# Optimization experiments

Measured on AMD Instinct MI355X. Metric: run time of the kernel, lower is better.

Reference implementation:

```python
import jax, jax.numpy as jnp
import numpy as np

N_NODES = 40000
N_EDGES = 320000
IN_DIM = 256
HID = 128
HEADS = 4
N_GAT = 3  # num_layers - 1
EPS = 1e-5
NEG_SLOPE = 0.2  # PyG GATConv default


def setup_inputs() -> dict:
    key = jax.random.key(0)
    ks = jax.random.split(key, 16)
    s = 0.05
    return {
        "x": jax.random.normal(ks[0], (N_NODES, IN_DIM), jnp.float32),
        "edge_index": jax.random.randint(ks[1], (2, N_EDGES), 0, N_NODES, jnp.int64),
        "proj_W": jax.random.normal(ks[2], (IN_DIM, HID), jnp.float32) * s,
        "proj_b": jnp.zeros((HID,), jnp.float32),
        "gat_W": jax.random.normal(ks[3], (N_GAT, HID, HEADS * HID), jnp.float32) * s,
        "gat_att_src": jax.random.normal(ks[4], (N_GAT, HEADS, HID), jnp.float32) * s,
        "gat_att_dst": jax.random.normal(ks[5], (N_GAT, HEADS, HID), jnp.float32) * s,
        "gat_bias": jnp.zeros((N_GAT, HID), jnp.float32),
        "ln_gamma": jnp.ones((N_GAT, HID), jnp.float32),
        "ln_beta": jnp.zeros((N_GAT, HID), jnp.float32),
        "gcn_W": jax.random.normal(ks[6], (HID, 1), jnp.float32) * s,
        "gcn_b": jnp.zeros((1,), jnp.float32),
    }


def reference(x, edge_index, proj_W, proj_b, gat_W, gat_att_src, gat_att_dst,
              gat_bias, ln_gamma, ln_beta, gcn_W, gcn_b):
    N = x.shape[0]
    loops = jnp.arange(N)
    src = jnp.concatenate([edge_index[0], loops])  # add_self_loops=True
    dst = jnp.concatenate([edge_index[1], loops])

    h = x @ proj_W + proj_b  # [N, HID]

    for i in range(N_GAT):
        identity = h
        xh = (h @ gat_W[i]).reshape(N, HEADS, HID)      # [N, H, C]
        a_s = jnp.einsum("nhc,hc->nh", xh, gat_att_src[i])  # [N, H]
        a_d = jnp.einsum("nhc,hc->nh", xh, gat_att_dst[i])
        e = jax.nn.leaky_relu(a_s[src] + a_d[dst], NEG_SLOPE)  # [E, H]
        # segment softmax over incoming edges per dst node
        m = jax.ops.segment_max(e, dst, num_segments=N)
        ex = jnp.exp(e - m[dst])
        denom = jax.ops.segment_sum(ex, dst, num_segments=N)
        alpha = ex / denom[dst]                         # [E, H]
        agg = jax.ops.segment_sum(xh[src] * alpha[:, :, None], dst, num_segments=N)
        h = agg.mean(axis=1) + gat_bias[i]              # concat=False -> head mean
        # LayerNorm (biased variance, eps=1e-5)
        mu = h.mean(-1, keepdims=True)
        var = ((h - mu) ** 2).mean(-1, keepdims=True)
        h = (h - mu) * jax.lax.rsqrt(var + EPS) * ln_gamma[i] + ln_beta[i]
        h = jax.nn.relu(h)
        # dropout: inference mode -> identity
        h = h + identity

    # GCNConv(hidden, 1) with symmetric normalization and self loops
    deg = jax.ops.segment_sum(jnp.ones_like(dst, dtype=h.dtype), dst, num_segments=N)
    dinv = jax.lax.rsqrt(deg)  # deg >= 1 due to self loops
    norm = dinv[src] * dinv[dst]                        # [E]
    xw = h @ gcn_W                                      # [N, 1]
    out = jax.ops.segment_sum(xw[src] * norm[:, None], dst, num_segments=N) + gcn_b
    return jax.nn.sigmoid(out).reshape(-1)
```

## Files before the change

### kernel.cpp

```cpp
#include <hip/hip_runtime.h>
#include <math.h>

#define INDIM 256
#define HID 128
#define HEADS 4
#define NGAT 3
#define LN_EPS 1e-5f
#define SLOPE 0.2f
#define MPAD 40064
#define LOG2E 1.4426950408889634f

typedef __attribute__((ext_vector_type(8))) short short8;
typedef __attribute__((ext_vector_type(4))) float f32x4;

__device__ inline float wsum(float v) {
#pragma unroll
  for (int m = 1; m < 64; m <<= 1) v += __shfl_xor(v, m, 64);
  return v;
}
__device__ inline float wmax(float v) {
#pragma unroll
  for (int m = 1; m < 64; m <<= 1) v = fmaxf(v, __shfl_xor(v, m, 64));
  return v;
}
__device__ inline float lk2(float v) { return fmaxf(v, SLOPE * v) * LOG2E; }
__device__ inline float sel4(float a0, float a1, float a2, float a3, int i) {
  float lo = (i & 1) ? a1 : a0;
  float hi = (i & 1) ? a3 : a2;
  return (i & 2) ? hi : lo;
}

__device__ inline unsigned short f2b(float f) {
  unsigned u = __float_as_uint(f);
  unsigned r = (u + 0x7FFFu + ((u >> 16) & 1u)) >> 16;
  return (unsigned short)r;
}
__device__ inline float b2f(unsigned short b) {
  return __uint_as_float(((unsigned)b) << 16);
}
__device__ inline void unp8(const uint4 v, float f[8]) {
  f[0] = __uint_as_float(v.x << 16);
  f[1] = __uint_as_float(v.x & 0xFFFF0000u);
  f[2] = __uint_as_float(v.y << 16);
  f[3] = __uint_as_float(v.y & 0xFFFF0000u);
  f[4] = __uint_as_float(v.z << 16);
  f[5] = __uint_as_float(v.z & 0xFFFF0000u);
  f[6] = __uint_as_float(v.w << 16);
  f[7] = __uint_as_float(v.w & 0xFFFF0000u);
}

__device__ __host__ inline size_t fidx(int row, int k, int K) {
  return ((size_t)(row >> 4) * (K >> 5) + (k >> 5)) * 512 +
         ((((k >> 3) & 3) * 16 + (row & 15)) << 3) + (k & 7);
}

__global__ void k_deg(const int* __restrict__ ei, int E, int N, int* __restrict__ deg) {
  int e = blockIdx.x * blockDim.x + threadIdx.x;
  if (e >= E + N) return;
  int dst = (e < E) ? ei[E + e] : (e - E);
  atomicAdd(&deg[dst], 1);
}

__global__ void k_scan1(const int* __restrict__ deg, int N, int* __restrict__ bsums) {
  __shared__ int s[256];
  int gid = blockIdx.x * 256 + threadIdx.x;
  s[threadIdx.x] = (gid < N) ? deg[gid] : 0;
  __syncthreads();
  for (int off = 128; off > 0; off >>= 1) {
    if (threadIdx.x < off) s[threadIdx.x] += s[threadIdx.x + off];
    __syncthreads();
  }
  if (threadIdx.x == 0) bsums[blockIdx.x] = s[0];
}

__global__ void k_scan2(int* __restrict__ bsums, int nblk, int* __restrict__ rowptr, int N) {
  __shared__ int s[256];
  int t = threadIdx.x;
  int v = (t < nblk) ? bsums[t] : 0;
  s[t] = v;
  __syncthreads();
  for (int off = 1; off < 256; off <<= 1) {
    int u = (t >= off) ? s[t - off] : 0;
    __syncthreads();
    s[t] += u;
    __syncthreads();
  }
  if (t < nblk) bsums[t] = s[t] - v;
  if (t == nblk - 1) rowptr[N] = s[t];
}

__global__ void k_scan3(const int* __restrict__ deg, int N, const int* __restrict__ bsums,
                        int* __restrict__ rowptr, int* __restrict__ cursor,
                        float* __restrict__ dinv) {
  __shared__ int s[256];
  int gid = blockIdx.x * 256 + threadIdx.x;
  int v = (gid < N) ? deg[gid] : 0;
  s[threadIdx.x] = v;
  __syncthreads();
  for (int off = 1; off < 256; off <<= 1) {
    int t = (threadIdx.x >= off) ? s[threadIdx.x - off] : 0;
    __syncthreads();
    s[threadIdx.x] += t;
    __syncthreads();
  }
  if (gid < N) {
    int ex = bsums[blockIdx.x] + s[threadIdx.x] - v;
    rowptr[gid] = ex;
    cursor[gid] = ex;
    dinv[gid] = rsqrtf((float)v);
  }
}

__global__ void k_fill(const int* __restrict__ ei, int E, int N,
                       int* __restrict__ cursor, int* __restrict__ csr) {
  int e = blockIdx.x * blockDim.x + threadIdx.x;
  if (e >= E + N) return;
  int src, dst;
  if (e < E) { src = ei[e]; dst = ei[E + e]; } else { src = dst = e - E; }
  int pos = atomicAdd(&cursor[dst], 1);
  csr[pos] = src;
}

__global__ void k_wprep(const float* __restrict__ Wp, const float* __restrict__ Wg,
                        unsigned short* __restrict__ WtPF,
                        unsigned short* __restrict__ Wt2F) {
  int idx = blockIdx.x * 256 + threadIdx.x;
  if (idx < INDIM * HID) {
    int k = idx >> 7, c = idx & 127;
    WtPF[fidx(c, k, INDIM)] = f2b(Wp[idx]);
    return;
  }
  idx -= INDIM * HID;
  if (idx >= NGAT * HID * HEADS * HID) return;
  int l = idx / (HID * HEADS * HID);
  int rem = idx - l * HID * HEADS * HID;
  int k = rem >> 9;
  int cc = rem & 511;
  int hh = cc >> 7, c = cc & 127;
  Wt2F[(size_t)l * (HID * HEADS * HID) + fidx(c, hh * HID + k, HEADS * HID)] =
      f2b(Wg[idx] * 0.25f);
}

__global__ void k_wvec(const float* __restrict__ W, const float* __restrict__ atts,
                       const float* __restrict__ attd, float* __restrict__ w_s,
                       float* __restrict__ w_d) {
  int lane = threadIdx.x & 63;
  int idx = blockIdx.x * 4 + (threadIdx.x >> 6);
  if (idx >= NGAT * HEADS * HID) return;
  int l = idx / (HEADS * HID);
  int rem = idx - l * (HEADS * HID);
  int hh = rem >> 7, k = rem & 127;
  const float2 w2 = *(const float2*)(W + ((size_t)(l * HID + k)) * (HEADS * HID) +
                                     hh * HID + lane * 2);
  const float2 s2 = *(const float2*)(atts + (size_t)(l * HEADS + hh) * HID + lane * 2);
  const float2 d2 = *(const float2*)(attd + (size_t)(l * HEADS + hh) * HID + lane * 2);
  float ps = w2.x * s2.x + w2.y * s2.y;
  float pd = w2.x * d2.x + w2.y * d2.y;
  ps = wsum(ps);
  pd = wsum(pd);
  if (lane == 0) { w_s[idx] = ps; w_d[idx] = pd; }
}

__global__ __launch_bounds__(256) void k_mm(
    const float* __restrict__ x, const unsigned short* __restrict__ WtPF,
    const float* __restrict__ bias, const float* __restrict__ ws0,
    const float* __restrict__ wd0, unsigned short* __restrict__ hb,
    float* __restrict__ a_s, float* __restrict__ a_d, int Mreal) {
  __shared__ unsigned short As[64 * INDIM];
  const int wid = threadIdx.x >> 6;
  const int lane = threadIdx.x & 63;
  const int l15 = lane & 15;
  const int g = lane >> 4;
  const int row0 = blockIdx.x * 64 + wid * 16;
#pragma unroll
  for (int i = 0; i < 8; ++i) {
    int p = threadIdx.x + 256 * i;
    int nl = p >> 5, kc = p & 31;
    int grow = blockIdx.x * 64 + nl;
    uint4 pk = make_uint4(0, 0, 0, 0);
    if (grow < Mreal) {
      const float* ap = x + (size_t)grow * INDIM + kc * 8;
      float4 u = *(const float4*)ap;
      float4 v = *(const float4*)(ap + 4);
      pk.x = (unsigned)f2b(u.x) | ((unsigned)f2b(u.y) << 16);
      pk.y = (unsigned)f2b(u.z) | ((unsigned)f2b(u.w) << 16);
      pk.z = (unsigned)f2b(v.x) | ((unsigned)f2b(v.y) << 16);
      pk.w = (unsigned)f2b(v.z) | ((unsigned)f2b(v.w) << 16);
    }
    *(uint4*)&As[((nl >> 4) * 8 + (kc >> 2)) * 512 + (((kc & 3) * 16 + (nl & 15)) << 3)] = pk;
  }
  __syncthreads();
  f32x4 acc[8] = {};
  const unsigned short* Bp = WtPF + lane * 8;
  for (int kb = 0; kb < 8; ++kb) {
    short8 af = *(const short8*)&As[(wid * 8 + kb) * 512 + lane * 8];
    short8 bfr[8];
#pragma unroll
    for (int ni = 0; ni < 8; ++ni)
      bfr[ni] = *(const short8*)(Bp + (size_t)(ni * 8 + kb) * 512);
#pragma unroll
    for (int ni = 0; ni < 8; ++ni)
      acc[ni] = __builtin_amdgcn_mfma_f32_16x16x32_bf16(af, bfr[ni], acc[ni], 0, 0, 0);
  }
#pragma unroll
  for (int r = 0; r < 4; ++r) {
    const int row = row0 + g * 4 + r;
    unsigned short* hbr = hb + (size_t)row * HID;
    float yv[8];
#pragma unroll
    for (int ni = 0; ni < 8; ++ni) {
      const int c = ni * 16 + l15;
      yv[ni] = acc[ni][r] + bias[c];
      hbr[c] = f2b(yv[ni]);
    }
    float ps[4], pd[4];
#pragma unroll
    for (int h4 = 0; h4 < 4; ++h4) {
      float pv = 0.f, qv = 0.f;
#pragma unroll
      for (int ni = 0; ni < 8; ++ni) {
        const int c = h4 * HID + ni * 16 + l15;
        pv = fmaf(yv[ni], ws0[c], pv);
        qv = fmaf(yv[ni], wd0[c], qv);
      }
#pragma unroll
      for (int m = 1; m < 16; m <<= 1) {
        pv += __shfl_xor(pv, m, 64);
        qv += __shfl_xor(qv, m, 64);
      }
      ps[h4] = pv;
      pd[h4] = qv;
    }
    if (l15 == 0) {
      *(float4*)(a_s + (size_t)row * 4) = make_float4(ps[0], ps[1], ps[2], ps[3]);
      *(float4*)(a_d + (size_t)row * 4) = make_float4(pd[0], pd[1], pd[2], pd[3]);
    }
  }
}

__global__ __launch_bounds__(256) void k_agg2(
    const int* __restrict__ rowptr, const int* __restrict__ csr,
    const unsigned short* __restrict__ hb, const float* __restrict__ a_s,
    const float* __restrict__ a_d, unsigned short* __restrict__ aggF, int N) {
  __shared__ int s_lds[4][64];
  __shared__ float al_lds[4][4][68];
  int lane = threadIdx.x & 63;
  int wid = threadIdx.x >> 6;
  int n = blockIdx.x * 4 + wid;
  if (n >= MPAD) return;
  const int g = lane >> 4;
  const int l15 = lane & 15;
  size_t oaddr = ((size_t)(n >> 4) * 16 + (g * 4 + (l15 >> 2))) * 512 +
                 (((l15 & 3) * 16 + (n & 15)) << 3);
  if (n >= N) {
    *(uint4*)(aggF + oaddr) = make_uint4(0, 0, 0, 0);
    return;
  }
  int beg = rowptr[n], end = rowptr[n + 1];
  int deg = end - beg;
  const unsigned short* hbase = hb + l15 * 8;
  float acc[8] = {};
  float f[8];
  if (deg <= 64) {
    const float ad = a_d[n * 4 + g];
    int sj[4];
    float ex[4];
    float mymax = -3e38f;
#pragma unroll
    for (int j = 0; j < 4; ++j) {
      int e = beg + l15 + 16 * j;
      bool v = e < end;
      int s = v ? csr[e] : 0;
      sj[j] = s;
      float Lv = v ? lk2(a_s[s * 4 + g] + ad) : -3e38f;
      ex[j] = Lv;
      mymax = fmaxf(mymax, Lv);
    }
#pragma unroll
    for (int m = 1; m < 16; m <<= 1) mymax = fmaxf(mymax, __shfl_xor(mymax, m, 64));
    float mysum = 0.f;
#pragma unroll
    for (int j = 0; j < 4; ++j) {
      ex[j] = exp2f(ex[j] - mymax);
      mysum += ex[j];
    }
#pragma unroll
    for (int m = 1; m < 16; m <<= 1) mysum += __shfl_xor(mysum, m, 64);
    float r = 1.f / mysum;
#pragma unroll
    for (int j = 0; j < 4; ++j) {
      int i = l15 + 16 * j;
      al_lds[wid][g][i] = ex[j] * r;
      if (g == 0) s_lds[wid][i] = sj[j];
    }
    asm volatile("s_waitcnt lgkmcnt(0)" ::: "memory");
    const int* sw = s_lds[wid];
    const float* aw = al_lds[wid][g];
    int nIter = (deg + 3) >> 2;
    for (int it = 0; it < nIter; ++it) {
      int4 s4 = *(const int4*)(sw + it * 4);
      float4 a4 = *(const float4*)(aw + it * 4);
      uint4 r0 = *(const uint4*)(hbase + (size_t)s4.x * HID);
      uint4 r1 = *(const uint4*)(hbase + (size_t)s4.y * HID);
      uint4 r2 = *(const uint4*)(hbase + (size_t)s4.z * HID);
      uint4 r3 = *(const uint4*)(hbase + (size_t)s4.w * HID);
      unp8(r0, f);
#pragma unroll
      for (int j = 0; j < 8; ++j) acc[j] = fmaf(a4.x, f[j], acc[j]);
      unp8(r1, f);
#pragma unroll
      for (int j = 0; j < 8; ++j) acc[j] = fmaf(a4.y, f[j], acc[j]);
      unp8(r2, f);
#pragma unroll
      for (int j = 0; j < 8; ++j) acc[j] = fmaf(a4.z, f[j], acc[j]);
      unp8(r3, f);
#pragma unroll
      for (int j = 0; j < 8; ++j) acc[j] = fmaf(a4.w, f[j], acc[j]);
    }
  } else {
    const float4 adv = *(const float4*)(a_d + (size_t)n * 4);
    float m0 = -3e38f, m1 = -3e38f, m2 = -3e38f, m3 = -3e38f;
    for (int e = beg + lane; e < end; e += 64) {
      int s = csr[e];
      const float4 asv = *(const float4*)(a_s + (size_t)s * 4);
      m0 = fmaxf(m0, lk2(asv.x + adv.x));
      m1 = fmaxf(m1, lk2(asv.y + adv.y));
      m2 = fmaxf(m2, lk2(asv.z + adv.z));
      m3 = fmaxf(m3, lk2(asv.w + adv.w));
    }
    m0 = wmax(m0); m1 = wmax(m1); m2 = wmax(m2); m3 = wmax(m3);
    float d0 = 0.f, d1 = 0.f, d2 = 0.f, d3 = 0.f;
    for (int e = beg + lane; e < end; e += 64) {
      int s = csr[e];
      const float4 asv = *(const float4*)(a_s + (size_t)s * 4);
      d0 += exp2f(lk2(asv.x + adv.x) - m0);
      d1 += exp2f(lk2(asv.y + adv.y) - m1);
      d2 += exp2f(lk2(asv.z + adv.z) - m2);
      d3 += exp2f(lk2(asv.w + adv.w) - m3);
    }
    float r0 = 1.f / wsum(d0);
    float r1 = 1.f / wsum(d1);
    float r2 = 1.f / wsum(d2);
    float r3 = 1.f / wsum(d3);
    for (int sb = beg; sb < end; sb += 64) {
      int e = sb + lane;
      bool val = e < end;
      int s = csr[val ? e : end - 1];
      const float4 asv = *(const float4*)(a_s + (size_t)s * 4);
      float q0 = val ? exp2f(lk2(asv.x + adv.x) - m0) * r0 : 0.f;
      float q1 = val ? exp2f(lk2(asv.y + adv.y) - m1) * r1 : 0.f;
      float q2 = val ? exp2f(lk2(asv.z + adv.z) - m2) * r2 : 0.f;
      float q3 = val ? exp2f(lk2(asv.w + adv.w) - m3) * r3 : 0.f;
      int cnt = min(64, end - sb);
      for (int i = 0; i < cnt; ++i) {
        int si = __shfl(s, i, 64);
        float c0 = __shfl(q0, i, 64), c1 = __shfl(q1, i, 64);
        float c2 = __shfl(q2, i, 64), c3 = __shfl(q3, i, 64);
        uint4 hv = *(const uint4*)(hbase + (size_t)si * HID);
        float bi = sel4(c0, c1, c2, c3, g);
        unp8(hv, f);
#pragma unroll
        for (int j = 0; j < 8; ++j) acc[j] = fmaf(bi, f[j], acc[j]);
      }
    }
  }
  uint4 pk;
  pk.x = (unsigned)f2b(acc[0]) | ((unsigned)f2b(acc[1]) << 16);
  pk.y = (unsigned)f2b(acc[2]) | ((unsigned)f2b(acc[3]) << 16);
  pk.z = (unsigned)f2b(acc[4]) | ((unsigned)f2b(acc[5]) << 16);
  pk.w = (unsigned)f2b(acc[6]) | ((unsigned)f2b(acc[7]) << 16);
  *(uint4*)(aggF + oaddr) = pk;
}

template <int ATT>
__global__ __launch_bounds__(256) void k_mm2(
    const unsigned short* __restrict__ aggF, const unsigned short* __restrict__ Bt,
    const float* __restrict__ bias, const float* __restrict__ gamma,
    const float* __restrict__ beta, const float* __restrict__ wsn,
    const float* __restrict__ wdn, unsigned short* __restrict__ hb,
    float* __restrict__ a_s, float* __restrict__ a_d,
    const float* __restrict__ dinvp, float* __restrict__ xwd) {
  const int wid = threadIdx.x >> 6;
  const int lane = threadIdx.x & 63;
  const int l15 = lane & 15;
  const int g = lane >> 4;
  const int row0 = blockIdx.x * 64 + wid * 16;
  f32x4 acc[8] = {};
  const unsigned short* Ap = aggF + (size_t)(row0 >> 4) * 16 * 512 + lane * 8;
  const unsigned short* Bp = Bt + lane * 8;
  for (int kb = 0; kb < 16; ++kb) {
    short8 a0 = *(const short8*)(Ap + kb * 512);
    short8 bfr[8];
#pragma unroll
    for (int ni = 0; ni < 8; ++ni)
      bfr[ni] = *(const short8*)(Bp + (size_t)(ni * 16 + kb) * 512);
#pragma unroll
    for (int ni = 0; ni < 8; ++ni)
      acc[ni] = __builtin_amdgcn_mfma_f32_16x16x32_bf16(a0, bfr[ni], acc[ni], 0, 0, 0);
  }
  float gm[8], bt8[8];
#pragma unroll
  for (int ni = 0; ni < 8; ++ni) {
    int c = ni * 16 + l15;
    gm[ni] = gamma[c];
    bt8[ni] = beta[c];
    float bs = bias[c];
#pragma unroll
    for (int r = 0; r < 4; ++r) acc[ni][r] += bs;
  }
#pragma unroll
  for (int r = 0; r < 4; ++r) {
    float s = 0.f;
#pragma unroll
    for (int ni = 0; ni < 8; ++ni) s += acc[ni][r];
#pragma unroll
    for (int m = 1; m < 16; m <<= 1) s += __shfl_xor(s, m, 64);
    float mu = s * (1.f / 128.f);
    float q = 0.f;
#pragma unroll
    for (int ni = 0; ni < 8; ++ni) {
      float dd = acc[ni][r] - mu;
      q += dd * dd;
    }
#pragma unroll
    for (int m = 1; m < 16; m <<= 1) q += __shfl_xor(q, m, 64);
    float rstd = rsqrtf(q * (1.f / 128.f) + LN_EPS);
    const int row = row0 + g * 4 + r;
    unsigned short* hbr = hb + (size_t)row * HID;
    float yv[8];
#pragma unroll
    for (int ni = 0; ni < 8; ++ni) {
      int c = ni * 16 + l15;
      float y = (acc[ni][r] - mu) * rstd * gm[ni] + bt8[ni];
      y = fmaxf(y, 0.f) + b2f(hbr[c]);
      hbr[c] = f2b(y);
      yv[ni] = y;
    }
    if (ATT == 1) {
      float ps[4], pd[4];
#pragma unroll
      for (int h4 = 0; h4 < 4; ++h4) {
        float pv = 0.f, qv = 0.f;
#pragma unroll
        for (int ni = 0; ni < 8; ++ni) {
          const int c = h4 * HID + ni * 16 + l15;
          pv = fmaf(yv[ni], wsn[c], pv);
          qv = fmaf(yv[ni], wdn[c], qv);
        }
#pragma unroll
        for (int m = 1; m < 16; m <<= 1) {
          pv += __shfl_xor(pv, m, 64);
          qv += __shfl_xor(qv, m, 64);
        }
        ps[h4] = pv;
        pd[h4] = qv;
      }
      if (l15 == 0) {
        *(float4*)(a_s + (size_t)row * 4) = make_float4(ps[0], ps[1], ps[2], ps[3]);
        *(float4*)(a_d + (size_t)row * 4) = make_float4(pd[0], pd[1], pd[2], pd[3]);
      }
    } else {
      float pv = 0.f;
#pragma unroll
      for (int ni = 0; ni < 8; ++ni) pv = fmaf(yv[ni], wsn[ni * 16 + l15], pv);
#pragma unroll
      for (int m = 1; m < 16; m <<= 1) pv += __shfl_xor(pv, m, 64);
      if (l15 == 0) xwd[row] = pv * dinvp[row];
    }
  }
}

__global__ __launch_bounds__(256) void k_gcn(const int* __restrict__ rowptr,
                                             const int* __restrict__ csr,
                                             const float* __restrict__ xwd,
                                             const float* __restrict__ dinv,
                                             const float* __restrict__ gcn_b,
                                             float* __restrict__ out, int N) {
  int n = blockIdx.x * blockDim.x + threadIdx.x;
  if (n >= N) return;
  float acc = 0.f;
  int beg = rowptr[n], end = rowptr[n + 1];
  int e = beg;
  for (; e + 4 <= end; e += 4) {
    int s0 = csr[e], s1 = csr[e + 1], s2 = csr[e + 2], s3 = csr[e + 3];
    float v0 = xwd[s0], v1 = xwd[s1], v2 = xwd[s2], v3 = xwd[s3];
    acc += (v0 + v1) + (v2 + v3);
  }
  for (; e < end; ++e) acc += xwd[csr[e]];
  float z = acc * dinv[n] + gcn_b[0];
  out[n] = 1.f / (1.f + expf(-z));
}

extern "C" void kernel_launch(void* const* d_in, const int* in_sizes, int n_in,
                              void* d_out, int out_size, void* d_ws, size_t ws_size,
                              hipStream_t stream) {
  const float* x = (const float*)d_in[0];
  const int* ei = (const int*)d_in[1];
  const float* proj_W = (const float*)d_in[2];
  const float* proj_b = (const float*)d_in[3];
  const float* gat_W = (const float*)d_in[4];
  const float* gat_as = (const float*)d_in[5];
  const float* gat_ad = (const float*)d_in[6];
  const float* gat_bias = (const float*)d_in[7];
  const float* ln_g = (const float*)d_in[8];
  const float* ln_b = (const float*)d_in[9];
  const float* gcn_W = (const float*)d_in[10];
  const float* gcn_b = (const float*)d_in[11];
  float* out = (float*)d_out;

  const int N = in_sizes[0] / INDIM;
  const int E = in_sizes[1] / 2;
  const int TOT = E + N;

  size_t off = 0;
  auto alloc = [&](size_t bytes) {
    void* p = (char*)d_ws + off;
    off += (bytes + 255) & ~(size_t)255;
    return p;
  };
  unsigned short* hb = (unsigned short*)alloc((size_t)MPAD * HID * 2);
  unsigned short* aggF = (unsigned short*)alloc((size_t)MPAD * HEADS * HID * 2);
  unsigned short* WtPF = (unsigned short*)alloc((size_t)HID * INDIM * 2);
  unsigned short* Wt2F = (unsigned short*)alloc((size_t)NGAT * HID * HEADS * HID * 2);
  float* w_s = (float*)alloc((size_t)NGAT * HEADS * HID * 4);
  float* w_d = (float*)alloc((size_t)NGAT * HEADS * HID * 4);
  float* a_s = (float*)alloc((size_t)MPAD * HEADS * 4);
  float* a_d = (float*)alloc((size_t)MPAD * HEADS * 4);
  int* deg = (int*)alloc((size_t)N * 4);
  int* rowptr = (int*)alloc((size_t)(N + 1) * 4);
  int* cursor = (int*)alloc((size_t)N * 4);
  int* csr = (int*)alloc((size_t)TOT * 4);
  int* bsums = (int*)alloc(1024);
  float* dinv = (float*)alloc((size_t)MPAD * 4);
  float* xwd = (float*)alloc((size_t)MPAD * 4);
  (void)ws_size;

  const int NBLK = (N + 255) / 256;
  const int EBLK = (TOT + 255) / 256;

  hipMemsetAsync(deg, 0, (size_t)N * 4, stream);
  k_deg<<<EBLK, 256, 0, stream>>>(ei, E, N, deg);
  k_scan1<<<NBLK, 256, 0, stream>>>(deg, N, bsums);
  k_scan2<<<1, 256, 0, stream>>>(bsums, NBLK, rowptr, N);
  k_scan3<<<NBLK, 256, 0, stream>>>(deg, N, bsums, rowptr, cursor, dinv);
  k_fill<<<EBLK, 256, 0, stream>>>(ei, E, N, cursor, csr);

  const int WPN = INDIM * HID + NGAT * HID * HEADS * HID;
  k_wprep<<<(WPN + 255) / 256, 256, 0, stream>>>(proj_W, gat_W, WtPF, Wt2F);
  k_wvec<<<(NGAT * HEADS * HID + 3) / 4, 256, 0, stream>>>(gat_W, gat_as, gat_ad, w_s, w_d);

  k_mm<<<MPAD / 64, 256, 0, stream>>>(x, WtPF, proj_b, w_s, w_d, hb, a_s, a_d, N);

  for (int i = 0; i < NGAT; ++i) {
    k_agg2<<<MPAD / 4, 256, 0, stream>>>(rowptr, csr, hb, a_s, a_d, aggF, N);
    if (i < NGAT - 1) {
      k_mm2<1><<<MPAD / 64, 256, 0, stream>>>(
          aggF, Wt2F + (size_t)i * HID * HEADS * HID, gat_bias + (size_t)i * HID,
          ln_g + (size_t)i * HID, ln_b + (size_t)i * HID,
          w_s + (size_t)(i + 1) * HEADS * HID, w_d + (size_t)(i + 1) * HEADS * HID,
          hb, a_s, a_d, nullptr, nullptr);
    } else {
      k_mm2<2><<<MPAD / 64, 256, 0, stream>>>(
          aggF, Wt2F + (size_t)i * HID * HEADS * HID, gat_bias + (size_t)i * HID,
          ln_g + (size_t)i * HID, ln_b + (size_t)i * HID, gcn_W, nullptr,
          hb, nullptr, nullptr, dinv, xwd);
    }
  }

  k_gcn<<<NBLK, 256, 0, stream>>>(rowptr, csr, xwd, dinv, gcn_b, out, N);
}
```

Baseline: 271.3 us.

## Split K across waves in k_mm2 with LDS reduction and vectorized epilogue

```diff
diff --git a/kernel.cpp b/kernel.cpp
--- a/kernel.cpp
+++ b/kernel.cpp
@@ -380,16 +380,19 @@
     const float* __restrict__ wdn, unsigned short* __restrict__ hb,
     float* __restrict__ a_s, float* __restrict__ a_d,
     const float* __restrict__ dinvp, float* __restrict__ xwd) {
+  __shared__ float red[4][16][132];
   const int wid = threadIdx.x >> 6;
   const int lane = threadIdx.x & 63;
   const int l15 = lane & 15;
   const int g = lane >> 4;
-  const int row0 = blockIdx.x * 64 + wid * 16;
+  const int row0 = blockIdx.x * 16;
   f32x4 acc[8] = {};
-  const unsigned short* Ap = aggF + (size_t)(row0 >> 4) * 16 * 512 + lane * 8;
+  const unsigned short* Ap = aggF + (size_t)blockIdx.x * 16 * 512 + lane * 8;
   const unsigned short* Bp = Bt + lane * 8;
-  for (int kb = 0; kb < 16; ++kb) {
-    short8 a0 = *(const short8*)(Ap + kb * 512);
+#pragma unroll
+  for (int kq = 0; kq < 4; ++kq) {
+    const int kb = wid * 4 + kq;
+    short8 a0 = *(const short8*)(Ap + (size_t)kb * 512);
     short8 bfr[8];
 #pragma unroll
     for (int ni = 0; ni < 8; ++ni)
@@ -398,75 +401,82 @@
     for (int ni = 0; ni < 8; ++ni)
       acc[ni] = __builtin_amdgcn_mfma_f32_16x16x32_bf16(a0, bfr[ni], acc[ni], 0, 0, 0);
   }
-  float gm[8], bt8[8];
-#pragma unroll
-  for (int ni = 0; ni < 8; ++ni) {
-    int c = ni * 16 + l15;
-    gm[ni] = gamma[c];
-    bt8[ni] = beta[c];
-    float bs = bias[c];
-#pragma unroll
-    for (int r = 0; r < 4; ++r) acc[ni][r] += bs;
-  }
-#pragma unroll
-  for (int r = 0; r < 4; ++r) {
-    float s = 0.f;
-#pragma unroll
-    for (int ni = 0; ni < 8; ++ni) s += acc[ni][r];
-#pragma unroll
-    for (int m = 1; m < 16; m <<= 1) s += __shfl_xor(s, m, 64);
-    float mu = s * (1.f / 128.f);
-    float q = 0.f;
-#pragma unroll
-    for (int ni = 0; ni < 8; ++ni) {
-      float dd = acc[ni][r] - mu;
-      q += dd * dd;
-    }
-#pragma unroll
-    for (int m = 1; m < 16; m <<= 1) q += __shfl_xor(q, m, 64);
-    float rstd = rsqrtf(q * (1.f / 128.f) + LN_EPS);
-    const int row = row0 + g * 4 + r;
-    unsigned short* hbr = hb + (size_t)row * HID;
-    float yv[8];
-#pragma unroll
-    for (int ni = 0; ni < 8; ++ni) {
-      int c = ni * 16 + l15;
-      float y = (acc[ni][r] - mu) * rstd * gm[ni] + bt8[ni];
-      y = fmaxf(y, 0.f) + b2f(hbr[c]);
-      hbr[c] = f2b(y);
-      yv[ni] = y;
-    }
-    if (ATT == 1) {
-      float ps[4], pd[4];
-#pragma unroll
-      for (int h4 = 0; h4 < 4; ++h4) {
-        float pv = 0.f, qv = 0.f;
-#pragma unroll
-        for (int ni = 0; ni < 8; ++ni) {
-          const int c = h4 * HID + ni * 16 + l15;
-          pv = fmaf(yv[ni], wsn[c], pv);
-          qv = fmaf(yv[ni], wdn[c], qv);
-        }
-#pragma unroll
-        for (int m = 1; m < 16; m <<= 1) {
-          pv += __shfl_xor(pv, m, 64);
-          qv += __shfl_xor(qv, m, 64);
-        }
-        ps[h4] = pv;
-        pd[h4] = qv;
+#pragma unroll
+  for (int ni = 0; ni < 8; ++ni)
+#pragma unroll
+    for (int r = 0; r < 4; ++r)
+      red[wid][g * 4 + r][ni * 16 + l15] = acc[ni][r];
+  __syncthreads();
+  const int row_l = threadIdx.x >> 4;
+  const int cg = threadIdx.x & 15;
+  const int c0 = cg * 8;
+  const int row = row0 + row_l;
+  float y[8];
+#pragma unroll
+  for (int j = 0; j < 8; ++j)
+    y[j] = ((red[0][row_l][c0 + j] + red[1][row_l][c0 + j]) +
+            (red[2][row_l][c0 + j] + red[3][row_l][c0 + j])) + bias[c0 + j];
+  float s = 0.f;
+#pragma unroll
+  for (int j = 0; j < 8; ++j) s += y[j];
+#pragma unroll
+  for (int m = 1; m < 16; m <<= 1) s += __shfl_xor(s, m, 64);
+  float mu = s * (1.f / 128.f);
+  float q = 0.f;
+#pragma unroll
+  for (int j = 0; j < 8; ++j) {
+    float dd = y[j] - mu;
+    q += dd * dd;
+  }
+#pragma unroll
+  for (int m = 1; m < 16; m <<= 1) q += __shfl_xor(q, m, 64);
+  float rstd = rsqrtf(q * (1.f / 128.f) + LN_EPS);
+  unsigned short* hbr = hb + (size_t)row * HID;
+  uint4 hv = *(const uint4*)(hbr + c0);
+  float res[8];
+  unp8(hv, res);
+  float yv[8];
+#pragma unroll
+  for (int j = 0; j < 8; ++j) {
+    float t = (y[j] - mu) * rstd * gamma[c0 + j] + beta[c0 + j];
+    yv[j] = fmaxf(t, 0.f) + res[j];
+  }
+  uint4 pk;
+  pk.x = (unsigned)f2b(yv[0]) | ((unsigned)f2b(yv[1]) << 16);
+  pk.y = (unsigned)f2b(yv[2]) | ((unsigned)f2b(yv[3]) << 16);
+  pk.z = (unsigned)f2b(yv[4]) | ((unsigned)f2b(yv[5]) << 16);
+  pk.w = (unsigned)f2b(yv[6]) | ((unsigned)f2b(yv[7]) << 16);
+  *(uint4*)(hbr + c0) = pk;
+  if (ATT == 1) {
+    float ps[4], pd[4];
+#pragma unroll
+    for (int h4 = 0; h4 < 4; ++h4) {
+      float pv = 0.f, qv = 0.f;
+#pragma unroll
+      for (int j = 0; j < 8; ++j) {
+        const int c = h4 * HID + c0 + j;
+        pv = fmaf(yv[j], wsn[c], pv);
+        qv = fmaf(yv[j], wdn[c], qv);
       }
-      if (l15 == 0) {
-        *(float4*)(a_s + (size_t)row * 4) = make_float4(ps[0], ps[1], ps[2], ps[3]);
-        *(float4*)(a_d + (size_t)row * 4) = make_float4(pd[0], pd[1], pd[2], pd[3]);
+#pragma unroll
+      for (int m = 1; m < 16; m <<= 1) {
+        pv += __shfl_xor(pv, m, 64);
+        qv += __shfl_xor(qv, m, 64);
       }
-    } else {
-      float pv = 0.f;
-#pragma unroll
-      for (int ni = 0; ni < 8; ++ni) pv = fmaf(yv[ni], wsn[ni * 16 + l15], pv);
-#pragma unroll
-      for (int m = 1; m < 16; m <<= 1) pv += __shfl_xor(pv, m, 64);
-      if (l15 == 0) xwd[row] = pv * dinvp[row];
-    }
+      ps[h4] = pv;
+      pd[h4] = qv;
+    }
+    if (cg == 0) {
+      *(float4*)(a_s + (size_t)row * 4) = make_float4(ps[0], ps[1], ps[2], ps[3]);
+      *(float4*)(a_d + (size_t)row * 4) = make_float4(pd[0], pd[1], pd[2], pd[3]);
+    }
+  } else {
+    float pv = 0.f;
+#pragma unroll
+    for (int j = 0; j < 8; ++j) pv = fmaf(yv[j], wsn[c0 + j], pv);
+#pragma unroll
+    for (int m = 1; m < 16; m <<= 1) pv += __shfl_xor(pv, m, 64);
+    if (cg == 0) xwd[row] = pv * dinvp[row];
   }
 }
 
@@ -554,13 +564,13 @@
   for (int i = 0; i < NGAT; ++i) {
     k_agg2<<<MPAD / 4, 256, 0, stream>>>(rowptr, csr, hb, a_s, a_d, aggF, N);
     if (i < NGAT - 1) {
-      k_mm2<1><<<MPAD / 64, 256, 0, stream>>>(
+      k_mm2<1><<<MPAD / 16, 256, 0, stream>>>(
           aggF, Wt2F + (size_t)i * HID * HEADS * HID, gat_bias + (size_t)i * HID,
           ln_g + (size_t)i * HID, ln_b + (size_t)i * HID,
           w_s + (size_t)(i + 1) * HEADS * HID, w_d + (size_t)(i + 1) * HEADS * HID,
           hb, a_s, a_d, nullptr, nullptr);
     } else {
-      k_mm2<2><<<MPAD / 64, 256, 0, stream>>>(
+      k_mm2<2><<<MPAD / 16, 256, 0, stream>>>(
           aggF, Wt2F + (size_t)i * HID * HEADS * HID, gat_bias + (size_t)i * HID,
           ln_g + (size_t)i * HID, ln_b + (size_t)i * HID, gcn_W, nullptr,
           hb, nullptr, nullptr, dinv, xwd);
```

Result: faster. 247.5 us (median of 2 runs) (-8.8%).
